# Kernel optimization log

Hardware: AMD Instinct MI355X
Metric: run time of the kernel (lower is better)

## Reference

```python
import jax, jax.numpy as jnp
import numpy as np

RMIN, RMAX = -5.0, 5.0
MIN_BIN, MIN_SLOPE = 1e-4, 1e-4
BATCH, DIM, NBINS, HID = 65536, 64, 8, 128
NLAYERS = 6
SPLIT = DIM // 2  # 32
PDIM = 3 * NBINS + 1  # 25


def _mlp(h, w1, c1, w2, c2, w3, c3, w4, c4):
    # equinox MLP, depth=3: relu on hidden layers, identity on output
    h = jax.nn.relu(h @ w1.T + c1)
    h = jax.nn.relu(h @ w2.T + c2)
    h = jax.nn.relu(h @ w3.T + c3)
    return h @ w4.T + c4


def _rqs_forward(x, params):
    # x: [B,T], params: [B,T,3K+1] -> (y, logdet) each [B,T]
    K = (params.shape[-1] - 1) // 3
    total = RMAX - RMIN
    widths = jax.nn.softmax(params[..., :K], axis=-1) * (total - K * MIN_BIN) + MIN_BIN
    heights = jax.nn.softmax(params[..., K:2 * K], axis=-1) * (total - K * MIN_BIN) + MIN_BIN
    slope_off = float(np.log(np.exp(1.0 - MIN_SLOPE) - 1.0))
    slopes = jax.nn.softplus(params[..., 2 * K:] + slope_off) + MIN_SLOPE  # [B,T,K+1]
    zero = jnp.zeros(widths.shape[:-1] + (1,), widths.dtype)
    x_pos = jnp.concatenate([zero, jnp.cumsum(widths, -1)], -1) + RMIN   # [B,T,K+1]
    y_pos = jnp.concatenate([zero, jnp.cumsum(heights, -1)], -1) + RMIN
    below, above = x < RMIN, x > RMAX
    sl, sr = slopes[..., 0], slopes[..., -1]
    y_lin_l = (x - RMIN) * sl + RMIN
    y_lin_r = (x - RMAX) * sr + RMAX
    # searchsorted(x_pos[1:-1], x, side='right') == count of knots <= x
    bin_idx = jnp.clip(jnp.sum(x_pos[..., 1:-1] <= x[..., None], axis=-1), 0, K - 1)
    take = lambda a, i: jnp.take_along_axis(a, i[..., None], axis=-1)[..., 0]
    x_k, x_k1 = take(x_pos, bin_idx), take(x_pos, bin_idx + 1)
    y_k, y_k1 = take(y_pos, bin_idx), take(y_pos, bin_idx + 1)
    d_k, d_k1 = take(slopes, bin_idx), take(slopes, bin_idx + 1)
    w, h = x_k1 - x_k, y_k1 - y_k
    xi = jnp.clip((x - x_k) / w, 0.0, 1.0)
    s = h / w
    xi1m = 1.0 - xi
    q = xi * xi1m
    num = s * xi * xi + d_k * q
    den = s + (d_k1 + d_k - 2.0 * s) * q
    y_sp = y_k + h * num / den
    deriv = s * s * (d_k1 * xi * xi + 2.0 * s * q + d_k * xi1m * xi1m) / (den * den)
    y = jnp.where(below, y_lin_l, jnp.where(above, y_lin_r, y_sp))
    ld = jnp.where(below, jnp.log(sl), jnp.where(above, jnp.log(sr), jnp.log(deriv)))
    return y, ld


def _coupling(x, w1, c1, w2, c2, w3, c3, w4, c4, midx, tidx):
    xm = x[:, midx]           # [B,32]
    xt = x[:, tidx]           # [B,32]
    params = _mlp(xm, w1, c1, w2, c2, w3, c3, w4, c4)  # [B, 32*25]
    params = params.reshape(xt.shape[0], xt.shape[1], PDIM)
    yt, ld = _rqs_forward(xt, params)
    y = jnp.zeros_like(x).at[:, midx].set(xm).at[:, tidx].set(yt)
    return y, jnp.sum(ld, axis=-1)


def _make_masks():
    half_m = np.arange(0, SPLIT, dtype=np.int32)          # mask==1 positions
    half_t = np.arange(SPLIT, DIM, dtype=np.int32)
    alt_m = np.arange(1, DIM, 2, dtype=np.int32)          # odd -> mask==1
    alt_t = np.arange(0, DIM, 2, dtype=np.int32)
    mi = np.stack([half_m if i % 2 == 0 else alt_m for i in range(NLAYERS)])
    ti = np.stack([half_t if i % 2 == 0 else alt_t for i in range(NLAYERS)])
    return jnp.asarray(mi), jnp.asarray(ti)


def setup_inputs() -> dict:
    key = jax.random.key(0)
    ks = jax.random.split(key, 10)
    sc = 0.05
    x = jax.random.normal(ks[0], (BATCH, DIM), jnp.float32)
    W1 = jax.random.normal(ks[1], (NLAYERS, HID, SPLIT), jnp.float32) * sc
    b1 = jax.random.normal(ks[2], (NLAYERS, HID), jnp.float32) * sc
    W2 = jax.random.normal(ks[3], (NLAYERS, HID, HID), jnp.float32) * sc
    b2 = jax.random.normal(ks[4], (NLAYERS, HID), jnp.float32) * sc
    W3 = jax.random.normal(ks[5], (NLAYERS, HID, HID), jnp.float32) * sc
    b3 = jax.random.normal(ks[6], (NLAYERS, HID), jnp.float32) * sc
    W4 = jax.random.normal(ks[7], (NLAYERS, SPLIT * PDIM, HID), jnp.float32) * sc
    b4 = jax.random.normal(ks[8], (NLAYERS, SPLIT * PDIM), jnp.float32) * sc
    mask_idx, transform_idx = _make_masks()
    return dict(x=x, W1=W1, b1=b1, W2=W2, b2=b2, W3=W3, b3=b3, W4=W4, b4=b4,
                mask_idx=mask_idx, transform_idx=transform_idx)


def reference(x, W1, b1, W2, b2, W3, b3, W4, b4, mask_idx, transform_idx):
    def step(carry, layer):
        xc, tot = carry
        w1, c1, w2, c2, w3, c3, w4, c4, mi, ti = layer
        y, ld = _coupling(xc, w1, c1, w2, c2, w3, c3, w4, c4, mi, ti)
        return (y, tot + ld), None
    init = (x, jnp.zeros(x.shape[0], x.dtype))
    (y, total_logdet), _ = jax.lax.scan(
        step, init, (W1, b1, W2, b2, W3, b3, W4, b4, mask_idx, transform_idx))
    return y, total_logdet
```

## Files before the change

### kernel.cpp

```cpp
#include <hip/hip_runtime.h>
#include <math.h>

#define BATCH   65536
#define DIM     64
#define HID     128
#define SPLIT   32
#define NBINS   8
#define PDIM    25
#define NLAYERS 6
#define R_MIN   (-5.0f)
#define R_MAX   (5.0f)
#define MIN_BIN   1.0e-4f
#define MIN_SLOPE 1.0e-4f
#define SOFF      0.54116666f

#define ROWSW 16
#define WAVES 4
#define MBLK  64
#define NT    256

#define N_W1  (HID*SPLIT)
#define N_W2  (HID*HID)
#define N_W4P (32*32*HID)
#define N_W4  (SPLIT*PDIM*HID)

typedef __attribute__((ext_vector_type(8))) short bf16x8;
typedef __attribute__((ext_vector_type(4))) float f32x4;

__device__ __forceinline__ short f2bf(float f) {
    unsigned u = __builtin_bit_cast(unsigned, f);
    unsigned r = u + 0x7FFFu + ((u >> 16) & 1u);
    return (short)(r >> 16);
}

__device__ __forceinline__ bf16x8 cvt8(const float* src) {
    float4 u = reinterpret_cast<const float4*>(src)[0];
    float4 v = reinterpret_cast<const float4*>(src)[1];
    bf16x8 a;
    a[0]=f2bf(u.x); a[1]=f2bf(u.y); a[2]=f2bf(u.z); a[3]=f2bf(u.w);
    a[4]=f2bf(v.x); a[5]=f2bf(v.y); a[6]=f2bf(v.z); a[7]=f2bf(v.w);
    return a;
}

__global__ void cvt_weights(const float* __restrict__ W1, const float* __restrict__ W2,
                            const float* __restrict__ W3, const float* __restrict__ W4,
                            short* __restrict__ o1, short* __restrict__ o2,
                            short* __restrict__ o3, short* __restrict__ o4) {
    const int stride = gridDim.x * blockDim.x;
    const int i0 = blockIdx.x * blockDim.x + threadIdx.x;
    for (int i = i0; i < NLAYERS*N_W1; i += stride) {
        const int L = i >> 12, rem = i & 4095;
        const int nt = rem >> 9, q = rem & 511;
        const int l = q >> 3, e = q & 7;
        o1[i] = f2bf(W1[L*N_W1 + (nt*16 + (l&15))*SPLIT + (l>>4)*8 + e]);
    }
    for (int i = i0; i < NLAYERS*N_W2; i += stride) {
        const int L = i >> 14, rem = i & 16383;
        const int c = rem >> 9, q = rem & 511;
        const int nt = c >> 2, kt = c & 3;
        const int l = q >> 3, e = q & 7;
        const int src = L*N_W2 + (nt*16 + (l&15))*HID + kt*32 + (l>>4)*8 + e;
        o2[i] = f2bf(W2[src]);
        o3[i] = f2bf(W3[src]);
    }
    for (int i = i0; i < NLAYERS*N_W4P; i += stride) {
        const int L = i >> 17, rem = i & (N_W4P - 1);
        const int c = rem >> 9, q = rem & 511;
        const int t = c >> 3, h = (c >> 2) & 1, kt = c & 3;
        const int l = q >> 3, e = q & 7;
        const int pp = h*16 + (l & 15);
        o4[i] = (pp < PDIM)
              ? f2bf(W4[(size_t)L*N_W4 + (size_t)(t*PDIM + pp)*HID + kt*32 + (l>>4)*8 + e])
              : (short)0;
    }
}

__global__ __launch_bounds__(NT, 2) void flow_layer(
    const float* xin, float* yout, float* logdet, const int first,
    const short* __restrict__ bW1, const float* __restrict__ b1,
    const short* __restrict__ bW2, const float* __restrict__ b2,
    const short* __restrict__ bW3, const float* __restrict__ b3,
    const short* __restrict__ bW4, const float* __restrict__ b4,
    const int* __restrict__ mi, const int* __restrict__ ti)
{
    __shared__ alignas(16) float pool[WAVES * ROWSW * 132];
    __shared__ float xts[WAVES][ROWSW][36];

    const int tid = threadIdx.x;
    const int w   = tid >> 6;
    const int l   = tid & 63;
    const int lr  = l & 15;
    const int lg  = l >> 4;
    const int rbase = blockIdx.x * MBLK + w * ROWSW;

    float* const actw = &pool[(w * ROWSW) * 132];

    {
        const int kcol = l & 31;
        const int mc = mi[kcol], tc = ti[kcol];
        const int r0 = l >> 5;
        #pragma unroll
        for (int it = 0; it < 8; ++it) {
            const int r = r0 + it * 2;
            const float* row = xin + (size_t)(rbase + r) * DIM;
            const float mv = row[mc];
            actw[r * 132 + kcol] = mv;
            xts[w][r][kcol] = row[tc];
            if (first) yout[(size_t)(rbase + r) * DIM + mc] = mv;
        }
    }

    {
        bf16x8 a0 = cvt8(&actw[lr * 132 + lg * 8]);
        f32x4 c[8];
        #pragma unroll
        for (int nt = 0; nt < 8; ++nt) { const float bv = b1[nt*16 + lr]; c[nt] = (f32x4){bv,bv,bv,bv}; }
        #pragma unroll
        for (int nt = 0; nt < 8; ++nt) {
            const bf16x8 bfr = *reinterpret_cast<const bf16x8*>(bW1 + (size_t)nt*512 + l*8);
            c[nt] = __builtin_amdgcn_mfma_f32_16x16x32_bf16(a0, bfr, c[nt], 0, 0, 0);
        }
        #pragma unroll
        for (int nt = 0; nt < 8; ++nt)
            #pragma unroll
            for (int j = 0; j < 4; ++j)
                actw[(lg*4 + j) * 132 + nt*16 + lr] = fmaxf(c[nt][j], 0.0f);
    }

    {
        bf16x8 a[4];
        #pragma unroll
        for (int kt = 0; kt < 4; ++kt) a[kt] = cvt8(&actw[lr * 132 + kt*32 + lg*8]);
        f32x4 c[8];
        #pragma unroll
        for (int nt = 0; nt < 8; ++nt) { const float bv = b2[nt*16 + lr]; c[nt] = (f32x4){bv,bv,bv,bv}; }
        #pragma unroll
        for (int kt = 0; kt < 4; ++kt)
            #pragma unroll
            for (int nt = 0; nt < 8; ++nt) {
                const bf16x8 bfr = *reinterpret_cast<const bf16x8*>(bW2 + (size_t)(nt*4 + kt)*512 + l*8);
                c[nt] = __builtin_amdgcn_mfma_f32_16x16x32_bf16(a[kt], bfr, c[nt], 0, 0, 0);
            }
        #pragma unroll
        for (int nt = 0; nt < 8; ++nt)
            #pragma unroll
            for (int j = 0; j < 4; ++j)
                actw[(lg*4 + j) * 132 + nt*16 + lr] = fmaxf(c[nt][j], 0.0f);
    }

    {
        bf16x8 a[4];
        #pragma unroll
        for (int kt = 0; kt < 4; ++kt) a[kt] = cvt8(&actw[lr * 132 + kt*32 + lg*8]);
        f32x4 c[8];
        #pragma unroll
        for (int nt = 0; nt < 8; ++nt) { const float bv = b3[nt*16 + lr]; c[nt] = (f32x4){bv,bv,bv,bv}; }
        #pragma unroll
        for (int kt = 0; kt < 4; ++kt)
            #pragma unroll
            for (int nt = 0; nt < 8; ++nt) {
                const bf16x8 bfr = *reinterpret_cast<const bf16x8*>(bW3 + (size_t)(nt*4 + kt)*512 + l*8);
                c[nt] = __builtin_amdgcn_mfma_f32_16x16x32_bf16(a[kt], bfr, c[nt], 0, 0, 0);
            }
        #pragma unroll
        for (int nt = 0; nt < 8; ++nt)
            #pragma unroll
            for (int j = 0; j < 4; ++j)
                actw[(lg*4 + j) * 132 + nt*16 + lr] = fmaxf(c[nt][j], 0.0f);
    }

    bf16x8 a4[4];
    #pragma unroll
    for (int kt = 0; kt < 4; ++kt) a4[kt] = cvt8(&actw[lr * 132 + kt*32 + lg*8]);

    float ldacc = 0.0f;
    #pragma unroll 1
    for (int tb = 0; tb < 8; ++tb) {
        f32x4 c[4][2];
        #pragma unroll
        for (int tl = 0; tl < 4; ++tl)
            #pragma unroll
            for (int h = 0; h < 2; ++h) {
                const int pp = h*16 + lr;
                const int t  = tb*4 + tl;
                const float bv = (pp < PDIM) ? b4[t*PDIM + pp] : 0.0f;
                c[tl][h] = (f32x4){bv, bv, bv, bv};
            }
        #pragma unroll
        for (int kt = 0; kt < 4; ++kt)
            #pragma unroll
            for (int tl = 0; tl < 4; ++tl)
                #pragma unroll
                for (int h = 0; h < 2; ++h) {
                    const bf16x8 bfr = *reinterpret_cast<const bf16x8*>(
                        bW4 + (size_t)((tb*4 + tl)*8 + h*4 + kt)*512 + l*8);
                    c[tl][h] = __builtin_amdgcn_mfma_f32_16x16x32_bf16(a4[kt], bfr, c[tl][h], 0, 0, 0);
                }
        #pragma unroll
        for (int tl = 0; tl < 4; ++tl)
            #pragma unroll
            for (int h = 0; h < 2; ++h)
                #pragma unroll
                for (int j = 0; j < 4; ++j)
                    actw[(lg*4 + j) * 132 + tl*33 + h*16 + lr] = c[tl][h][j];

        const float* prow = &actw[lr * 132 + lg * 33];

        float sl[NBINS + 1];
        #pragma unroll
        for (int i = 0; i < NBINS + 1; ++i) {
            const float z = prow[2*NBINS + i] + SOFF;
            const float sp = (z > 15.0f) ? z : __logf(1.0f + __expf(z));
            sl[i] = sp + MIN_SLOPE;
        }

        float wd[NBINS];
        {
            float q[NBINS];
            #pragma unroll
            for (int i = 0; i < NBINS; ++i) q[i] = prow[i];
            float mx = q[0];
            #pragma unroll
            for (int i = 1; i < NBINS; ++i) mx = fmaxf(mx, q[i]);
            float sum = 0.0f;
            #pragma unroll
            for (int i = 0; i < NBINS; ++i) { wd[i] = __expf(q[i] - mx); sum += wd[i]; }
            const float sc = __fdividef((R_MAX - R_MIN) - NBINS * MIN_BIN, sum);
            #pragma unroll
            for (int i = 0; i < NBINS; ++i) wd[i] = wd[i] * sc + MIN_BIN;
        }
        float hg[NBINS];
        {
            float q[NBINS];
            #pragma unroll
            for (int i = 0; i < NBINS; ++i) q[i] = prow[NBINS + i];
            float mx = q[0];
            #pragma unroll
            for (int i = 1; i < NBINS; ++i) mx = fmaxf(mx, q[i]);
            float sum = 0.0f;
            #pragma unroll
            for (int i = 0; i < NBINS; ++i) { hg[i] = __expf(q[i] - mx); sum += hg[i]; }
            const float sc = __fdividef((R_MAX - R_MIN) - NBINS * MIN_BIN, sum);
            #pragma unroll
            for (int i = 0; i < NBINS; ++i) hg[i] = hg[i] * sc + MIN_BIN;
        }

        const float x = xts[w][lr][tb*4 + lg];

        int b = 0;
        {
            float cx = R_MIN;
            #pragma unroll
            for (int i = 1; i < NBINS; ++i) { cx += wd[i-1]; b += (cx <= x) ? 1 : 0; }
        }
        float x_k = R_MIN, y_k = R_MIN, wsel = wd[0], hsel = hg[0], d_k = sl[0], d_k1 = sl[1];
        {
            float cx = R_MIN, cy = R_MIN;
            #pragma unroll
            for (int i = 0; i < NBINS; ++i) {
                if (i == b) { x_k = cx; y_k = cy; wsel = wd[i]; hsel = hg[i];
                              d_k = sl[i]; d_k1 = sl[i+1]; }
                cx += wd[i]; cy += hg[i];
            }
        }

        const float invw = __fdividef(1.0f, wsel);
        float xi = (x - x_k) * invw;
        xi = fminf(fmaxf(xi, 0.0f), 1.0f);
        const float s    = hsel * invw;
        const float xi1m = 1.0f - xi;
        const float q    = xi * xi1m;
        const float num  = s * xi * xi + d_k * q;
        const float den  = s + (d_k1 + d_k - 2.0f * s) * q;
        const float invden = __fdividef(1.0f, den);
        const float y_sp = y_k + hsel * num * invden;
        const float deriv = s * s * (d_k1 * xi * xi + 2.0f * s * q + d_k * xi1m * xi1m)
                            * invden * invden;

        const bool below = x < R_MIN;
        const bool above = x > R_MAX;
        const float yv = below ? ((x - R_MIN) * sl[0]     + R_MIN)
                       : (above ? ((x - R_MAX) * sl[NBINS] + R_MAX) : y_sp);
        const float dv = below ? sl[0] : (above ? sl[NBINS] : deriv);
        ldacc += __logf(dv);

        yout[(size_t)(rbase + lr) * DIM + ti[tb*4 + lg]] = yv;
    }

    ldacc += __shfl_xor(ldacc, 16, 64);
    ldacc += __shfl_xor(ldacc, 32, 64);
    if (l < 16) {
        const int row = rbase + lr;
        if (first) logdet[row] = ldacc;
        else       logdet[row] += ldacc;
    }
}

extern "C" void kernel_launch(void* const* d_in, const int* in_sizes, int n_in,
                              void* d_out, int out_size, void* d_ws, size_t ws_size,
                              hipStream_t stream) {
    const float* x  = (const float*)d_in[0];
    const float* W1 = (const float*)d_in[1];
    const float* b1 = (const float*)d_in[2];
    const float* W2 = (const float*)d_in[3];
    const float* b2 = (const float*)d_in[4];
    const float* W3 = (const float*)d_in[5];
    const float* b3 = (const float*)d_in[6];
    const float* W4 = (const float*)d_in[7];
    const float* b4 = (const float*)d_in[8];
    const int*   mi = (const int*)d_in[9];
    const int*   ti = (const int*)d_in[10];

    float* y      = (float*)d_out;
    float* logdet = y + (size_t)BATCH * DIM;

    short* bW1 = (short*)d_ws;
    short* bW2 = bW1 + NLAYERS * N_W1;
    short* bW3 = bW2 + NLAYERS * N_W2;
    short* bW4 = bW3 + NLAYERS * N_W2;

    cvt_weights<<<512, 256, 0, stream>>>(W1, W2, W3, W4, bW1, bW2, bW3, bW4);

    dim3 grid(BATCH / MBLK), block(NT);
    for (int L = 0; L < NLAYERS; ++L) {
        flow_layer<<<grid, block, 0, stream>>>(
            (L == 0) ? x : y, y, logdet, (L == 0) ? 1 : 0,
            bW1 + (size_t)L * N_W1, b1 + L * HID,
            bW2 + (size_t)L * N_W2, b2 + L * HID,
            bW3 + (size_t)L * N_W2, b3 + L * HID,
            bW4 + (size_t)L * N_W4P, b4 + (size_t)L * SPLIT * PDIM,
            mi + L * SPLIT, ti + L * SPLIT);
    }
}
```

Baseline: 384.5 us.

## Transpose MFMA operands, give each wave 32 rows, keep bf16 activations in LDS

Each wave now handles 32 rows instead of 16, so every weight fragment loaded from global memory feeds two MFMAs and weight traffic per row is halved. Operands are swapped to compute the transposed product. Activations are stored in LDS as packed bf16 using the v_cvt_pk_bf16_f32 instruction, which removes the per-fragment float-to-bf16 conversion. The final-layer parameters now come straight from registers through a reorganised W4 layout and a padded bias array, with no LDS round-trip. The cost is more accumulator registers per thread and fewer threads per block, which may reduce occupancy and latency hiding.

```diff
diff --git a/kernel.cpp b/kernel.cpp
--- a/kernel.cpp
+++ b/kernel.cpp
@@ -14,10 +14,10 @@
 #define MIN_SLOPE 1.0e-4f
 #define SOFF      0.54116666f
 
-#define ROWSW 16
-#define WAVES 4
+#define ROWSW 32
+#define WAVES 2
 #define MBLK  64
-#define NT    256
+#define NT    128
 
 #define N_W1  (HID*SPLIT)
 #define N_W2  (HID*HID)
@@ -33,19 +33,27 @@
     return (short)(r >> 16);
 }
 
-__device__ __forceinline__ bf16x8 cvt8(const float* src) {
-    float4 u = reinterpret_cast<const float4*>(src)[0];
-    float4 v = reinterpret_cast<const float4*>(src)[1];
+__device__ __forceinline__ unsigned pk2(float a, float b) {
+    unsigned r;
+    asm("v_cvt_pk_bf16_f32 %0, %1, %2" : "=v"(r) : "v"(a), "v"(b));
+    return r;
+}
+
+__device__ __forceinline__ bf16x8 ldfrag(const short* base) {
+    short4 lo = *reinterpret_cast<const short4*>(base);
+    short4 hi = *reinterpret_cast<const short4*>(base + 128);
     bf16x8 a;
-    a[0]=f2bf(u.x); a[1]=f2bf(u.y); a[2]=f2bf(u.z); a[3]=f2bf(u.w);
-    a[4]=f2bf(v.x); a[5]=f2bf(v.y); a[6]=f2bf(v.z); a[7]=f2bf(v.w);
+    a[0]=lo.x; a[1]=lo.y; a[2]=lo.z; a[3]=lo.w;
+    a[4]=hi.x; a[5]=hi.y; a[6]=hi.z; a[7]=hi.w;
     return a;
 }
 
 __global__ void cvt_weights(const float* __restrict__ W1, const float* __restrict__ W2,
                             const float* __restrict__ W3, const float* __restrict__ W4,
+                            const float* __restrict__ b4,
                             short* __restrict__ o1, short* __restrict__ o2,
-                            short* __restrict__ o3, short* __restrict__ o4) {
+                            short* __restrict__ o3, short* __restrict__ o4,
+                            float* __restrict__ b4q) {
     const int stride = gridDim.x * blockDim.x;
     const int i0 = blockIdx.x * blockDim.x + threadIdx.x;
     for (int i = i0; i < NLAYERS*N_W1; i += stride) {
@@ -66,233 +74,244 @@
     for (int i = i0; i < NLAYERS*N_W4P; i += stride) {
         const int L = i >> 17, rem = i & (N_W4P - 1);
         const int c = rem >> 9, q = rem & 511;
-        const int t = c >> 3, h = (c >> 2) & 1, kt = c & 3;
+        const int tb = c >> 5, pq = (c >> 2) & 7, kt = c & 3;
         const int l = q >> 3, e = q & 7;
-        const int pp = h*16 + (l & 15);
-        o4[i] = (pp < PDIM)
-              ? f2bf(W4[(size_t)L*N_W4 + (size_t)(t*PDIM + pp)*HID + kt*32 + (l>>4)*8 + e])
+        const int t = tb*4 + ((l & 15) >> 2);
+        const int p = pq*4 + (l & 3);
+        o4[i] = (p < PDIM)
+              ? f2bf(W4[(size_t)L*N_W4 + (size_t)(t*PDIM + p)*HID + kt*32 + (l>>4)*8 + e])
               : (short)0;
     }
-}
-
-__global__ __launch_bounds__(NT, 2) void flow_layer(
+    for (int i = i0; i < NLAYERS*SPLIT*32; i += stride) {
+        const int L = i >> 10, rem = i & 1023;
+        const int t = rem >> 5, p = rem & 31;
+        b4q[i] = (p < PDIM) ? b4[L*SPLIT*PDIM + t*PDIM + p] : 0.0f;
+    }
+}
+
+__global__ __launch_bounds__(NT, 3) void flow_layer(
     const float* xin, float* yout, float* logdet, const int first,
     const short* __restrict__ bW1, const float* __restrict__ b1,
     const short* __restrict__ bW2, const float* __restrict__ b2,
     const short* __restrict__ bW3, const float* __restrict__ b3,
-    const short* __restrict__ bW4, const float* __restrict__ b4,
+    const short* __restrict__ bW4, const float* __restrict__ b4q,
     const int* __restrict__ mi, const int* __restrict__ ti)
 {
-    __shared__ alignas(16) float pool[WAVES * ROWSW * 132];
-    __shared__ float xts[WAVES][ROWSW][36];
+    __shared__ short act[WAVES][32 * 128];
+    __shared__ float xts[WAVES][ROWSW][33];
 
     const int tid = threadIdx.x;
-    const int w   = tid >> 6;
+    const int wv  = tid >> 6;
     const int l   = tid & 63;
     const int lr  = l & 15;
     const int lg  = l >> 4;
-    const int rbase = blockIdx.x * MBLK + w * ROWSW;
-
-    float* const actw = &pool[(w * ROWSW) * 132];
+    const int rbase = blockIdx.x * MBLK + wv * ROWSW;
+
+    short* const actw = &act[wv][0];
 
     {
         const int kcol = l & 31;
         const int mc = mi[kcol], tc = ti[kcol];
         const int r0 = l >> 5;
         #pragma unroll
-        for (int it = 0; it < 8; ++it) {
+        for (int it = 0; it < 16; ++it) {
             const int r = r0 + it * 2;
             const float* row = xin + (size_t)(rbase + r) * DIM;
             const float mv = row[mc];
-            actw[r * 132 + kcol] = mv;
-            xts[w][r][kcol] = row[tc];
+            actw[(kcol >> 2)*128 + r*4 + (kcol & 3)] = f2bf(mv);
+            xts[wv][r][kcol] = row[tc];
             if (first) yout[(size_t)(rbase + r) * DIM + mc] = mv;
         }
     }
 
     {
-        bf16x8 a0 = cvt8(&actw[lr * 132 + lg * 8]);
-        f32x4 c[8];
-        #pragma unroll
-        for (int nt = 0; nt < 8; ++nt) { const float bv = b1[nt*16 + lr]; c[nt] = (f32x4){bv,bv,bv,bv}; }
+        bf16x8 afr[2];
+        #pragma unroll
+        for (int rh = 0; rh < 2; ++rh)
+            afr[rh] = ldfrag(&actw[(2*lg)*128 + (lr + rh*16)*4]);
+        f32x4 c[8][2];
         #pragma unroll
         for (int nt = 0; nt < 8; ++nt) {
-            const bf16x8 bfr = *reinterpret_cast<const bf16x8*>(bW1 + (size_t)nt*512 + l*8);
-            c[nt] = __builtin_amdgcn_mfma_f32_16x16x32_bf16(a0, bfr, c[nt], 0, 0, 0);
+            const float4 bv = *reinterpret_cast<const float4*>(b1 + nt*16 + lg*4);
+            c[nt][0] = (f32x4){bv.x, bv.y, bv.z, bv.w};
+            c[nt][1] = c[nt][0];
+        }
+        #pragma unroll
+        for (int nt = 0; nt < 8; ++nt) {
+            const bf16x8 wfr = *reinterpret_cast<const bf16x8*>(bW1 + (size_t)nt*512 + l*8);
+            #pragma unroll
+            for (int rh = 0; rh < 2; ++rh)
+                c[nt][rh] = __builtin_amdgcn_mfma_f32_16x16x32_bf16(wfr, afr[rh], c[nt][rh], 0, 0, 0);
         }
         #pragma unroll
         for (int nt = 0; nt < 8; ++nt)
             #pragma unroll
-            for (int j = 0; j < 4; ++j)
-                actw[(lg*4 + j) * 132 + nt*16 + lr] = fmaxf(c[nt][j], 0.0f);
-    }
-
-    {
-        bf16x8 a[4];
-        #pragma unroll
-        for (int kt = 0; kt < 4; ++kt) a[kt] = cvt8(&actw[lr * 132 + kt*32 + lg*8]);
-        f32x4 c[8];
-        #pragma unroll
-        for (int nt = 0; nt < 8; ++nt) { const float bv = b2[nt*16 + lr]; c[nt] = (f32x4){bv,bv,bv,bv}; }
+            for (int rh = 0; rh < 2; ++rh) {
+                const unsigned u0 = pk2(fmaxf(c[nt][rh][0], 0.0f), fmaxf(c[nt][rh][1], 0.0f));
+                const unsigned u1 = pk2(fmaxf(c[nt][rh][2], 0.0f), fmaxf(c[nt][rh][3], 0.0f));
+                *reinterpret_cast<uint2*>(&actw[(nt*4 + lg)*128 + (lr + rh*16)*4]) = (uint2){u0, u1};
+            }
+    }
+
+    #pragma unroll 1
+    for (int ph = 0; ph < 2; ++ph) {
+        const short* Wp = ph ? bW3 : bW2;
+        const float* bp = ph ? b3  : b2;
+        bf16x8 afr[4][2];
         #pragma unroll
         for (int kt = 0; kt < 4; ++kt)
             #pragma unroll
+            for (int rh = 0; rh < 2; ++rh)
+                afr[kt][rh] = ldfrag(&actw[(kt*8 + 2*lg)*128 + (lr + rh*16)*4]);
+        f32x4 c[8][2];
+        #pragma unroll
+        for (int nt = 0; nt < 8; ++nt) {
+            const float4 bv = *reinterpret_cast<const float4*>(bp + nt*16 + lg*4);
+            c[nt][0] = (f32x4){bv.x, bv.y, bv.z, bv.w};
+            c[nt][1] = c[nt][0];
+        }
+        #pragma unroll
+        for (int kt = 0; kt < 4; ++kt)
+            #pragma unroll
             for (int nt = 0; nt < 8; ++nt) {
-                const bf16x8 bfr = *reinterpret_cast<const bf16x8*>(bW2 + (size_t)(nt*4 + kt)*512 + l*8);
-                c[nt] = __builtin_amdgcn_mfma_f32_16x16x32_bf16(a[kt], bfr, c[nt], 0, 0, 0);
+                const bf16x8 wfr = *reinterpret_cast<const bf16x8*>(Wp + (size_t)(nt*4 + kt)*512 + l*8);
+                #pragma unroll
+                for (int rh = 0; rh < 2; ++rh)
+                    c[nt][rh] = __builtin_amdgcn_mfma_f32_16x16x32_bf16(wfr, afr[kt][rh], c[nt][rh], 0, 0, 0);
             }
         #pragma unroll
         for (int nt = 0; nt < 8; ++nt)
             #pragma unroll
-            for (int j = 0; j < 4; ++j)
-                actw[(lg*4 + j) * 132 + nt*16 + lr] = fmaxf(c[nt][j], 0.0f);
-    }
-
-    {
-        bf16x8 a[4];
-        #pragma unroll
-        for (int kt = 0; kt < 4; ++kt) a[kt] = cvt8(&actw[lr * 132 + kt*32 + lg*8]);
-        f32x4 c[8];
-        #pragma unroll
-        for (int nt = 0; nt < 8; ++nt) { const float bv = b3[nt*16 + lr]; c[nt] = (f32x4){bv,bv,bv,bv}; }
-        #pragma unroll
-        for (int kt = 0; kt < 4; ++kt)
-            #pragma unroll
-            for (int nt = 0; nt < 8; ++nt) {
-                const bf16x8 bfr = *reinterpret_cast<const bf16x8*>(bW3 + (size_t)(nt*4 + kt)*512 + l*8);
-                c[nt] = __builtin_amdgcn_mfma_f32_16x16x32_bf16(a[kt], bfr, c[nt], 0, 0, 0);
-            }
-        #pragma unroll
-        for (int nt = 0; nt < 8; ++nt)
-            #pragma unroll
-            for (int j = 0; j < 4; ++j)
-                actw[(lg*4 + j) * 132 + nt*16 + lr] = fmaxf(c[nt][j], 0.0f);
-    }
-
-    bf16x8 a4[4];
+            for (int rh = 0; rh < 2; ++rh) {
+                const unsigned u0 = pk2(fmaxf(c[nt][rh][0], 0.0f), fmaxf(c[nt][rh][1], 0.0f));
+                const unsigned u1 = pk2(fmaxf(c[nt][rh][2], 0.0f), fmaxf(c[nt][rh][3], 0.0f));
+                *reinterpret_cast<uint2*>(&actw[(nt*4 + lg)*128 + (lr + rh*16)*4]) = (uint2){u0, u1};
+            }
+    }
+
+    bf16x8 afr[4][2];
     #pragma unroll
-    for (int kt = 0; kt < 4; ++kt) a4[kt] = cvt8(&actw[lr * 132 + kt*32 + lg*8]);
-
-    float ldacc = 0.0f;
+    for (int kt = 0; kt < 4; ++kt)
+        #pragma unroll
+        for (int rh = 0; rh < 2; ++rh)
+            afr[kt][rh] = ldfrag(&actw[(kt*8 + 2*lg)*128 + (lr + rh*16)*4]);
+
+    float ld0 = 0.0f, ld1 = 0.0f;
     #pragma unroll 1
     for (int tb = 0; tb < 8; ++tb) {
-        f32x4 c[4][2];
-        #pragma unroll
-        for (int tl = 0; tl < 4; ++tl)
-            #pragma unroll
-            for (int h = 0; h < 2; ++h) {
-                const int pp = h*16 + lr;
-                const int t  = tb*4 + tl;
-                const float bv = (pp < PDIM) ? b4[t*PDIM + pp] : 0.0f;
-                c[tl][h] = (f32x4){bv, bv, bv, bv};
-            }
+        const int t = tb*4 + lg;
+        f32x4 c[8][2];
+        #pragma unroll
+        for (int pq = 0; pq < 8; ++pq) {
+            const float4 bv = *reinterpret_cast<const float4*>(b4q + t*32 + pq*4);
+            c[pq][0] = (f32x4){bv.x, bv.y, bv.z, bv.w};
+            c[pq][1] = c[pq][0];
+        }
         #pragma unroll
         for (int kt = 0; kt < 4; ++kt)
             #pragma unroll
-            for (int tl = 0; tl < 4; ++tl)
-                #pragma unroll
-                for (int h = 0; h < 2; ++h) {
-                    const bf16x8 bfr = *reinterpret_cast<const bf16x8*>(
-                        bW4 + (size_t)((tb*4 + tl)*8 + h*4 + kt)*512 + l*8);
-                    c[tl][h] = __builtin_amdgcn_mfma_f32_16x16x32_bf16(a4[kt], bfr, c[tl][h], 0, 0, 0);
+            for (int pq = 0; pq < 8; ++pq) {
+                const bf16x8 wfr = *reinterpret_cast<const bf16x8*>(
+                    bW4 + (size_t)((tb*8 + pq)*4 + kt)*512 + l*8);
+                #pragma unroll
+                for (int rh = 0; rh < 2; ++rh)
+                    c[pq][rh] = __builtin_amdgcn_mfma_f32_16x16x32_bf16(wfr, afr[kt][rh], c[pq][rh], 0, 0, 0);
+            }
+
+        const int ticol = ti[t];
+        #pragma unroll
+        for (int rh = 0; rh < 2; ++rh) {
+            float p[32];
+            #pragma unroll
+            for (int pq = 0; pq < 8; ++pq)
+                #pragma unroll
+                for (int j = 0; j < 4; ++j) p[pq*4 + j] = c[pq][rh][j];
+
+            const int r = lr + rh*16;
+
+            float sl[NBINS + 1];
+            #pragma unroll
+            for (int i = 0; i < NBINS + 1; ++i) {
+                const float z = p[2*NBINS + i] + SOFF;
+                const float sp = (z > 15.0f) ? z : __logf(1.0f + __expf(z));
+                sl[i] = sp + MIN_SLOPE;
+            }
+            float wd[NBINS];
+            {
+                float mx = p[0];
+                #pragma unroll
+                for (int i = 1; i < NBINS; ++i) mx = fmaxf(mx, p[i]);
+                float sum = 0.0f;
+                #pragma unroll
+                for (int i = 0; i < NBINS; ++i) { wd[i] = __expf(p[i] - mx); sum += wd[i]; }
+                const float sc = __fdividef((R_MAX - R_MIN) - NBINS * MIN_BIN, sum);
+                #pragma unroll
+                for (int i = 0; i < NBINS; ++i) wd[i] = wd[i] * sc + MIN_BIN;
+            }
+            float hg[NBINS];
+            {
+                float mx = p[NBINS];
+                #pragma unroll
+                for (int i = 1; i < NBINS; ++i) mx = fmaxf(mx, p[NBINS + i]);
+                float sum = 0.0f;
+                #pragma unroll
+                for (int i = 0; i < NBINS; ++i) { hg[i] = __expf(p[NBINS + i] - mx); sum += hg[i]; }
+                const float sc = __fdividef((R_MAX - R_MIN) - NBINS * MIN_BIN, sum);
+                #pragma unroll
+                for (int i = 0; i < NBINS; ++i) hg[i] = hg[i] * sc + MIN_BIN;
+            }
+
+            const float x = xts[wv][r][t];
+
+            int b = 0;
+            {
+                float cx = R_MIN;
+                #pragma unroll
+                for (int i = 1; i < NBINS; ++i) { cx += wd[i-1]; b += (cx <= x) ? 1 : 0; }
+            }
+            float x_k = R_MIN, y_k = R_MIN, wsel = wd[0], hsel = hg[0], d_k = sl[0], d_k1 = sl[1];
+            {
+                float cx = R_MIN, cy = R_MIN;
+                #pragma unroll
+                for (int i = 0; i < NBINS; ++i) {
+                    if (i == b) { x_k = cx; y_k = cy; wsel = wd[i]; hsel = hg[i];
+                                  d_k = sl[i]; d_k1 = sl[i+1]; }
+                    cx += wd[i]; cy += hg[i];
                 }
-        #pragma unroll
-        for (int tl = 0; tl < 4; ++tl)
-            #pragma unroll
-            for (int h = 0; h < 2; ++h)
-                #pragma unroll
-                for (int j = 0; j < 4; ++j)
-                    actw[(lg*4 + j) * 132 + tl*33 + h*16 + lr] = c[tl][h][j];
-
-        const float* prow = &actw[lr * 132 + lg * 33];
-
-        float sl[NBINS + 1];
-        #pragma unroll
-        for (int i = 0; i < NBINS + 1; ++i) {
-            const float z = prow[2*NBINS + i] + SOFF;
-            const float sp = (z > 15.0f) ? z : __logf(1.0f + __expf(z));
-            sl[i] = sp + MIN_SLOPE;
-        }
-
-        float wd[NBINS];
-        {
-            float q[NBINS];
-            #pragma unroll
-            for (int i = 0; i < NBINS; ++i) q[i] = prow[i];
-            float mx = q[0];
-            #pragma unroll
-            for (int i = 1; i < NBINS; ++i) mx = fmaxf(mx, q[i]);
-            float sum = 0.0f;
-            #pragma unroll
-            for (int i = 0; i < NBINS; ++i) { wd[i] = __expf(q[i] - mx); sum += wd[i]; }
-            const float sc = __fdividef((R_MAX - R_MIN) - NBINS * MIN_BIN, sum);
-            #pragma unroll
-            for (int i = 0; i < NBINS; ++i) wd[i] = wd[i] * sc + MIN_BIN;
-        }
-        float hg[NBINS];
-        {
-            float q[NBINS];
-            #pragma unroll
-            for (int i = 0; i < NBINS; ++i) q[i] = prow[NBINS + i];
-            float mx = q[0];
-            #pragma unroll
-            for (int i = 1; i < NBINS; ++i) mx = fmaxf(mx, q[i]);
-            float sum = 0.0f;
-            #pragma unroll
-            for (int i = 0; i < NBINS; ++i) { hg[i] = __expf(q[i] - mx); sum += hg[i]; }
-            const float sc = __fdividef((R_MAX - R_MIN) - NBINS * MIN_BIN, sum);
-            #pragma unroll
-            for (int i = 0; i < NBINS; ++i) hg[i] = hg[i] * sc + MIN_BIN;
-        }
-
-        const float x = xts[w][lr][tb*4 + lg];
-
-        int b = 0;
-        {
-            float cx = R_MIN;
-            #pragma unroll
-            for (int i = 1; i < NBINS; ++i) { cx += wd[i-1]; b += (cx <= x) ? 1 : 0; }
-        }
-        float x_k = R_MIN, y_k = R_MIN, wsel = wd[0], hsel = hg[0], d_k = sl[0], d_k1 = sl[1];
-        {
-            float cx = R_MIN, cy = R_MIN;
-            #pragma unroll
-            for (int i = 0; i < NBINS; ++i) {
-                if (i == b) { x_k = cx; y_k = cy; wsel = wd[i]; hsel = hg[i];
-                              d_k = sl[i]; d_k1 = sl[i+1]; }
-                cx += wd[i]; cy += hg[i];
-            }
-        }
-
-        const float invw = __fdividef(1.0f, wsel);
-        float xi = (x - x_k) * invw;
-        xi = fminf(fmaxf(xi, 0.0f), 1.0f);
-        const float s    = hsel * invw;
-        const float xi1m = 1.0f - xi;
-        const float q    = xi * xi1m;
-        const float num  = s * xi * xi + d_k * q;
-        const float den  = s + (d_k1 + d_k - 2.0f * s) * q;
-        const float invden = __fdividef(1.0f, den);
-        const float y_sp = y_k + hsel * num * invden;
-        const float deriv = s * s * (d_k1 * xi * xi + 2.0f * s * q + d_k * xi1m * xi1m)
-                            * invden * invden;
-
-        const bool below = x < R_MIN;
-        const bool above = x > R_MAX;
-        const float yv = below ? ((x - R_MIN) * sl[0]     + R_MIN)
-                       : (above ? ((x - R_MAX) * sl[NBINS] + R_MAX) : y_sp);
-        const float dv = below ? sl[0] : (above ? sl[NBINS] : deriv);
-        ldacc += __logf(dv);
-
-        yout[(size_t)(rbase + lr) * DIM + ti[tb*4 + lg]] = yv;
-    }
-
-    ldacc += __shfl_xor(ldacc, 16, 64);
-    ldacc += __shfl_xor(ldacc, 32, 64);
+            }
+
+            const float invw = __fdividef(1.0f, wsel);
+            float xi = (x - x_k) * invw;
+            xi = fminf(fmaxf(xi, 0.0f), 1.0f);
+            const float s    = hsel * invw;
+            const float xi1m = 1.0f - xi;
+            const float q    = xi * xi1m;
+            const float num  = s * xi * xi + d_k * q;
+            const float den  = s + (d_k1 + d_k - 2.0f * s) * q;
+            const float invden = __fdividef(1.0f, den);
+            const float y_sp = y_k + hsel * num * invden;
+            const float deriv = s * s * (d_k1 * xi * xi + 2.0f * s * q + d_k * xi1m * xi1m)
+                                * invden * invden;
+
+            const bool below = x < R_MIN;
+            const bool above = x > R_MAX;
+            const float yv = below ? ((x - R_MIN) * sl[0]     + R_MIN)
+                           : (above ? ((x - R_MAX) * sl[NBINS] + R_MAX) : y_sp);
+            const float dv = below ? sl[0] : (above ? sl[NBINS] : deriv);
+            if (rh == 0) ld0 += __logf(dv); else ld1 += __logf(dv);
+
+            yout[(size_t)(rbase + r) * DIM + ticol] = yv;
+        }
+    }
+
+    ld0 += __shfl_xor(ld0, 16, 64);
+    ld0 += __shfl_xor(ld0, 32, 64);
+    ld1 += __shfl_xor(ld1, 16, 64);
+    ld1 += __shfl_xor(ld1, 32, 64);
     if (l < 16) {
-        const int row = rbase + lr;
-        if (first) logdet[row] = ldacc;
-        else       logdet[row] += ldacc;
+        const int row0 = rbase + lr;
+        if (first) { logdet[row0] = ld0; logdet[row0 + 16] = ld1; }
+        else       { logdet[row0] += ld0; logdet[row0 + 16] += ld1; }
     }
 }
 
@@ -318,8 +337,9 @@
     short* bW2 = bW1 + NLAYERS * N_W1;
     short* bW3 = bW2 + NLAYERS * N_W2;
     short* bW4 = bW3 + NLAYERS * N_W2;
-
-    cvt_weights<<<512, 256, 0, stream>>>(W1, W2, W3, W4, bW1, bW2, bW3, bW4);
+    float* b4q = (float*)(bW4 + (size_t)NLAYERS * N_W4P);
+
+    cvt_weights<<<512, 256, 0, stream>>>(W1, W2, W3, W4, b4, bW1, bW2, bW3, bW4, b4q);
 
     dim3 grid(BATCH / MBLK), block(NT);
     for (int L = 0; L < NLAYERS; ++L) {
@@ -328,7 +348,7 @@
             bW1 + (size_t)L * N_W1, b1 + L * HID,
             bW2 + (size_t)L * N_W2, b2 + L * HID,
             bW3 + (size_t)L * N_W2, b3 + L * HID,
-            bW4 + (size_t)L * N_W4P, b4 + (size_t)L * SPLIT * PDIM,
+            bW4 + (size_t)L * N_W4P, b4q + (size_t)L * SPLIT * 32,
             mi + L * SPLIT, ti + L * SPLIT);
     }
 }
```

Result: slower. 551.9 us (+43.5%).
